# Kernel tuning notes

Hardware: AMD Instinct MI355X
Metric: run time of the kernel (lower is better)

The kernel has to match this reference:

```python
import jax, jax.numpy as jnp
import numpy as np

NS = 100000; NT = 100000; M = 512; D = 256; DL = 128; H = 4; C = 256; K = 64
ITERS = 50; POS_MARGIN = 0.1


def conv1(w, b, x):
    # 1x1 Conv1d: x (B, Cin, N), w (Cout, Cin)
    return jnp.einsum('oi,bin->bon', w, x) + b[None, :, None]


def attn_block(p, x, src):
    # attentional propagation: MHA message + MLP([x, msg]) (residual added by caller)
    wq, bq, wk, bk, wv, bv, wm, bm, w1, b1, w2, b2 = p
    B, Dm, N = x.shape
    Dh = Dm // H
    Nm = src.shape[2]
    q = conv1(wq, bq, x).reshape(B, H, Dh, N)
    k = conv1(wk, bk, src).reshape(B, H, Dh, Nm)
    v = conv1(wv, bv, src).reshape(B, H, Dh, Nm)
    a = jax.nn.softmax(jnp.einsum('bhdn,bhdm->bhnm', q, k) * (1.0 / np.sqrt(Dh)), axis=-1)
    msg = jnp.einsum('bhnm,bhdm->bhdn', a, v).reshape(B, Dm, N)
    msg = conv1(wm, bm, msg)
    h = jax.nn.relu(conv1(w1, b1, jnp.concatenate([x, msg], axis=1)))
    return conv1(w2, b2, h)


def nn_id(points, nodes):
    # 1-NN node id per point; points (N,3), nodes (M,3)
    d = (jnp.sum(points * points, 1, keepdims=True) - 2.0 * points @ nodes.T
         + jnp.sum(nodes * nodes, 1)[None, :])
    return jnp.argmin(d, axis=1)


def build_patches(pcd_id, m, k):
    # grouping_wrapper: first k point indices assigned to each node, -1 padded
    n = pcd_id.shape[0]
    order = jnp.argsort(pcd_id)  # stable
    sid = pcd_id[order]
    starts = jnp.searchsorted(sid, jnp.arange(m))
    rank = jnp.arange(n) - starts[sid]
    patch = jnp.full((m, k), -1, jnp.int32)
    patch = patch.at[sid, rank].set(order.astype(jnp.int32), mode='drop')  # rank>=k dropped
    mask = (patch < 0).astype(jnp.float32)
    return jnp.where(patch < 0, 0, patch), mask


def log_optimal_transport(scores, alpha, iters):
    b, m, n = scores.shape
    bins0 = jnp.full((b, m, 1), alpha)
    bins1 = jnp.full((b, 1, n), alpha)
    corner = jnp.full((b, 1, 1), alpha)
    Z = jnp.concatenate([jnp.concatenate([scores, bins0], 2),
                         jnp.concatenate([bins1, corner], 2)], 1)
    norm = -np.log(m + n)
    log_mu = jnp.concatenate([jnp.full((m,), norm, jnp.float32), jnp.array([np.log(n) + norm], jnp.float32)])
    log_nu = jnp.concatenate([jnp.full((n,), norm, jnp.float32), jnp.array([np.log(m) + norm], jnp.float32)])
    log_mu = jnp.broadcast_to(log_mu, (b, m + 1))
    log_nu = jnp.broadcast_to(log_nu, (b, n + 1))

    def body(carry, _):
        u, v = carry
        u = log_mu - jax.nn.logsumexp(Z + v[:, None, :], axis=2)
        v = log_nu - jax.nn.logsumexp(Z + u[:, :, None], axis=1)
        return (u, v), None

    (u, v), _ = jax.lax.scan(body, (jnp.zeros((b, m + 1)), jnp.zeros((b, n + 1))), None, length=iters)
    return Z + u[:, :, None] + v[:, None, :] - norm


def rpmnet_sinkhorn(log_alpha, bins0, bins1, iters):
    b = log_alpha.shape[0]
    corner = jnp.zeros((b, 1, 1), log_alpha.dtype)
    la = jnp.concatenate([jnp.concatenate([log_alpha, bins0], 2),
                          jnp.concatenate([bins1, corner], 2)], 1)

    def body(la, _):
        row = la - jax.nn.logsumexp(la, axis=2, keepdims=True)
        la = jnp.concatenate([row[:, :-1, :], la[:, -1:, :]], axis=1)  # normalize all rows but slack
        col = la - jax.nn.logsumexp(la, axis=1, keepdims=True)
        la = jnp.concatenate([col[:, :, :-1], la[:, :, -1:]], axis=2)  # normalize all cols but slack
        return la, None

    la, _ = jax.lax.scan(body, la, None, length=iters)
    return la


def _forward(src_pcd_c, tgt_pcd_c, src_node_c, tgt_node_c, src_feats_c, tgt_feats_c,
             src_final_f, tgt_final_f, rot, trans, src_pcd_raw, tgt_pcd_raw,
             c_wq, c_bq, c_wk, c_bk, c_wv, c_bv, c_wm, c_bm, c_w1, c_b1, c_w2, c_b2,
             l_wq, l_bq, l_wk, l_bk, l_wv, l_bv, l_wm, l_bm, l_w1, l_b1, l_w2, l_b2,
             fp_w, fp_b, lfp_w, lfp_b, bin_score, node_corr):
    # KNN assignment + patch grouping (irregular gather/scatter)
    src_patch, src_mask = build_patches(nn_id(src_pcd_c, src_node_c), M, K)
    tgt_patch, tgt_mask = build_patches(nn_id(tgt_pcd_c, tgt_node_c), M, K)
    # coarse attention stack (self, cross, self) with residuals
    cp = lambda i: (c_wq[i], c_bq[i], c_wk[i], c_bk[i], c_wv[i], c_bv[i], c_wm[i], c_bm[i],
                    c_w1[i], c_b1[i], c_w2[i], c_b2[i])
    sf, tf = src_feats_c, tgt_feats_c
    sf = sf + attn_block(cp(0), sf, sf); tf = tf + attn_block(cp(0), tf, tf)
    sf = sf + attn_block(cp(1), sf, tf); tf = tf + attn_block(cp(1), tf, sf)  # sequential, like torch
    sf = sf + attn_block(cp(2), sf, sf); tf = tf + attn_block(cp(2), tf, tf)
    sf = conv1(fp_w, fp_b, sf); tf = conv1(fp_w, fp_b, tf)
    scores = jnp.einsum('bdn,bdm->bnm', sf, tf) / np.sqrt(D)
    scores = log_optimal_transport(scores, bin_score, ITERS)
    # correspondence-driven patch gather
    sn = node_corr[:, 0]; tn = node_corr[:, 1]
    src_sel = src_patch[sn].reshape(-1)
    tgt_sel = tgt_patch[tn].reshape(-1)
    smask = src_mask[sn]; tmask = tgt_mask[tn]  # (C,K)
    # GT local scores (training path)
    src_raw_t = (rot @ src_pcd_raw.T + trans).T
    sc = src_raw_t[src_sel].reshape(C, K, 3)
    tc = tgt_pcd_raw[tgt_sel].reshape(C, K, 3)
    d2 = jnp.maximum(jnp.sum(sc * sc, -1)[:, :, None] + jnp.sum(tc * tc, -1)[:, None, :]
                     - 2.0 * jnp.einsum('cnd,cmd->cnm', sc, tc), 0.0)
    gt = (jnp.sqrt(d2) < POS_MARGIN).astype(jnp.float32)
    row = jnp.maximum(1.0 - jnp.sum(gt, -1), 0.0)[:, :, None]
    col = jnp.maximum(1.0 - jnp.sum(gt, -2), 0.0)[:, None, :]
    col = jnp.concatenate([col, jnp.zeros((C, 1, 1), jnp.float32)], -1)
    gt = jnp.concatenate([jnp.concatenate([gt, row], -1), col], -2)  # (C,K+1,K+1)
    gt = gt.at[:, :-1, :].multiply(1.0 - smask[:, :, None])
    gt = gt.at[:, :, :-1].multiply(1.0 - tmask[:, None, :])
    # local patch features + attention stack
    spf = src_final_f[src_sel].reshape(C, K, DL).transpose(0, 2, 1)  # (C,DL,K)
    tpf = tgt_final_f[tgt_sel].reshape(C, K, DL).transpose(0, 2, 1)
    lp = lambda i: (l_wq[i], l_bq[i], l_wk[i], l_bk[i], l_wv[i], l_bv[i], l_wm[i], l_bm[i],
                    l_w1[i], l_b1[i], l_w2[i], l_b2[i])
    spf = spf + attn_block(lp(0), spf, spf); tpf = tpf + attn_block(lp(0), tpf, tpf)
    spf = spf + attn_block(lp(1), spf, tpf); tpf = tpf + attn_block(lp(1), tpf, spf)
    spf = spf + attn_block(lp(2), spf, spf); tpf = tpf + attn_block(lp(2), tpf, tpf)
    spf = conv1(lfp_w, lfp_b, spf); tpf = conv1(lfp_w, lfp_b, tpf)
    ls = jnp.einsum('bdn,bdm->bnm', spf, tpf) / np.sqrt(DL)
    ls = jnp.where(smask[:, :, None] > 0, -1e6, ls)
    ls = jnp.where(tmask[:, None, :] > 0, -1e6, ls)
    ls = rpmnet_sinkhorn(ls, jnp.zeros((C, K, 1), jnp.float32), jnp.zeros((C, 1, K), jnp.float32), ITERS)
    return scores, ls, gt


def setup_inputs() -> dict:
    key = jax.random.key(0)
    ks = jax.random.split(key, 48)

    def rn(i, shape, scale):
        return jax.random.normal(ks[i], shape, jnp.float32) * scale

    inp = {}
    inp['src_pcd_c'] = jax.random.uniform(ks[0], (NS, 3), jnp.float32)
    inp['tgt_pcd_c'] = jax.random.uniform(ks[1], (NT, 3), jnp.float32)
    inp['src_node_c'] = jax.random.uniform(ks[2], (M, 3), jnp.float32)
    inp['tgt_node_c'] = jax.random.uniform(ks[3], (M, 3), jnp.float32)
    inp['src_feats_c'] = rn(4, (1, D, M), 1.0)
    inp['tgt_feats_c'] = rn(5, (1, D, M), 1.0)
    inp['src_final_f'] = rn(6, (NS, DL), 1.0)
    inp['tgt_final_f'] = rn(7, (NT, DL), 1.0)
    inp['rot'] = jnp.eye(3, dtype=jnp.float32)
    inp['trans'] = jnp.zeros((3, 1), jnp.float32)
    inp['src_pcd_raw'] = jax.random.uniform(ks[8], (NS, 3), jnp.float32)
    inp['tgt_pcd_raw'] = jax.random.uniform(ks[9], (NT, 3), jnp.float32)
    inp['node_corr'] = jax.random.randint(ks[10], (C, 2), 0, M)
    i = 11
    for pre, d in (('c_', D), ('l_', DL)):
        for nm in ('wq', 'wk', 'wv', 'wm'):
            inp[pre + nm] = rn(i, (3, d, d), 1.0 / np.sqrt(d)); i += 1
            inp[pre + 'b' + nm[1]] = jnp.zeros((3, d), jnp.float32)
        inp[pre + 'w1'] = rn(i, (3, 2 * d, 2 * d), 1.0 / np.sqrt(2 * d)); i += 1
        inp[pre + 'b1'] = jnp.zeros((3, 2 * d), jnp.float32)
        inp[pre + 'w2'] = rn(i, (3, d, 2 * d), 1.0 / np.sqrt(2 * d)); i += 1
        inp[pre + 'b2'] = jnp.zeros((3, d), jnp.float32)
    inp['fp_w'] = rn(i, (D, D), 1.0 / np.sqrt(D)); i += 1
    inp['fp_b'] = jnp.zeros((D,), jnp.float32)
    inp['lfp_w'] = rn(i, (DL, DL), 1.0 / np.sqrt(DL)); i += 1
    inp['lfp_b'] = jnp.zeros((DL,), jnp.float32)
    inp['bin_score'] = jnp.ones((), jnp.float32)
    return inp


def reference(src_pcd_c, tgt_pcd_c, src_node_c, tgt_node_c, src_feats_c, tgt_feats_c,
              src_final_f, tgt_final_f, rot, trans, src_pcd_raw, tgt_pcd_raw,
              c_wq, c_bq, c_wk, c_bk, c_wv, c_bv, c_wm, c_bm, c_w1, c_b1, c_w2, c_b2,
              l_wq, l_bq, l_wk, l_bk, l_wv, l_bv, l_wm, l_bm, l_w1, l_b1, l_w2, l_b2,
              fp_w, fp_b, lfp_w, lfp_b, bin_score, node_corr):
    return _forward(src_pcd_c, tgt_pcd_c, src_node_c, tgt_node_c, src_feats_c, tgt_feats_c,
                    src_final_f, tgt_final_f, rot, trans, src_pcd_raw, tgt_pcd_raw,
                    c_wq, c_bq, c_wk, c_bk, c_wv, c_bv, c_wm, c_bm, c_w1, c_b1, c_w2, c_b2,
                    l_wq, l_bq, l_wk, l_bk, l_wv, l_bv, l_wm, l_bm, l_w1, l_b1, l_w2, l_b2,
                    fp_w, fp_b, lfp_w, lfp_b, bin_score, node_corr)
```

## Files before the change

kernel.cpp:

```cpp
#include <hip/hip_runtime.h>
#include <math.h>

static constexpr int NODES = 512;
static constexpr int CC    = 256;
static constexpr int KP    = 64;
static constexpr int ZDIM  = 513;
static constexpr int TPNB  = 16;
static constexpr int TPROWS = 33;

typedef unsigned short u16;
typedef short bf16x8 __attribute__((ext_vector_type(8)));
typedef float f32x4 __attribute__((ext_vector_type(4)));

__device__ __forceinline__ u16 f2b(float f){
  unsigned u = __float_as_uint(f);
  unsigned r = (u + 0x7FFF + ((u >> 16) & 1)) >> 16;
  return (u16)r;
}
__device__ __forceinline__ float b2f(u16 h){ return __uint_as_float(((unsigned)h) << 16); }
__device__ __forceinline__ f32x4 mfma16(bf16x8 a, bf16x8 b, f32x4 c){
  return __builtin_amdgcn_mfma_f32_16x16x32_bf16(a, b, c, 0, 0, 0);
}
__device__ __forceinline__ void astore(float* p, float v){
  __hip_atomic_store(p, v, __ATOMIC_RELAXED, __HIP_MEMORY_SCOPE_AGENT);
}
__device__ __forceinline__ float fpoll(const float* p){
  const unsigned* up = (const unsigned*)p;
  unsigned v = __hip_atomic_load(up, __ATOMIC_RELAXED, __HIP_MEMORY_SCOPE_AGENT);
  while (v == 0xFFFFFFFFu){
    __builtin_amdgcn_s_sleep(1);
    v = __hip_atomic_load(up, __ATOMIC_RELAXED, __HIP_MEMORY_SCOPE_AGENT);
  }
  return __uint_as_float(v);
}
__device__ __forceinline__ void fpoll2(const float* p0, const float* p1,
                                       float* a, float* b){
  const unsigned* u0 = (const unsigned*)p0;
  const unsigned* u1 = (const unsigned*)p1;
  unsigned x = __hip_atomic_load(u0, __ATOMIC_RELAXED, __HIP_MEMORY_SCOPE_AGENT);
  unsigned y = __hip_atomic_load(u1, __ATOMIC_RELAXED, __HIP_MEMORY_SCOPE_AGENT);
  while (x == 0xFFFFFFFFu || y == 0xFFFFFFFFu){
    __builtin_amdgcn_s_sleep(1);
    if (x == 0xFFFFFFFFu) x = __hip_atomic_load(u0, __ATOMIC_RELAXED, __HIP_MEMORY_SCOPE_AGENT);
    if (y == 0xFFFFFFFFu) y = __hip_atomic_load(u1, __ATOMIC_RELAXED, __HIP_MEMORY_SCOPE_AGENT);
  }
  *a = __uint_as_float(x); *b = __uint_as_float(y);
}

static constexpr int NBW = (2539520 + 255) / 256;

__global__ __launch_bounds__(256) void prep(
  const float* cwq, const float* cwk, const float* cwv, const float* cwm,
  const float* cw1, const float* cw2, const float* fpw,
  const float* lwq, const float* lwk, const float* lwv, const float* lwm,
  const float* lw1, const float* lw2, const float* lfp, u16* __restrict__ dst,
  const float* __restrict__ pts_s, int ns, const float* __restrict__ nodes_s,
  int* __restrict__ id_s, int* __restrict__ hist_s,
  const float* __restrict__ pts_t, int ntt, const float* __restrict__ nodes_t,
  int* __restrict__ id_t, int* __restrict__ hist_t, int nbs, int nbnn,
  const float* __restrict__ fs, const float* __restrict__ ft,
  u16* __restrict__ cf, float* __restrict__ cff)
{
  int blk = blockIdx.x;
  int t = threadIdx.x;
  if (blk < NBW){
    int i = blk*256 + t;
    if (i >= 2539520) return;
    const float* s; int off;
    if      (i <  196608){ s=cwq; off=0; }
    else if (i <  393216){ s=cwk; off=196608; }
    else if (i <  589824){ s=cwv; off=393216; }
    else if (i <  786432){ s=cwm; off=589824; }
    else if (i < 1572864){ s=cw1; off=786432; }
    else if (i < 1966080){ s=cw2; off=1572864; }
    else if (i < 2031616){ s=fpw; off=1966080; }
    else if (i < 2080768){ s=lwq; off=2031616; }
    else if (i < 2129920){ s=lwk; off=2080768; }
    else if (i < 2179072){ s=lwv; off=2129920; }
    else if (i < 2228224){ s=lwm; off=2179072; }
    else if (i < 2424832){ s=lw1; off=2228224; }
    else if (i < 2523136){ s=lw2; off=2424832; }
    else                 { s=lfp; off=2523136; }
    dst[i] = f2b(s[i - off]);
    return;
  }
  if (blk < NBW + nbnn){
#pragma clang fp contract(off)
    __shared__ float nx[NODES], ny[NODES], nz[NODES], nn[NODES];
    __shared__ int h[NODES];
    int b2 = blk - NBW;
    const float* pts; const float* nodes; int* out; int* hist; int n; int bb;
    if (b2 < nbs){ pts=pts_s; nodes=nodes_s; out=id_s; hist=hist_s; n=ns; bb=b2; }
    else         { pts=pts_t; nodes=nodes_t; out=id_t; hist=hist_t; n=ntt; bb=b2-nbs; }
    for (int m = t; m < NODES; m += 256){
      float a = nodes[m*3+0], b = nodes[m*3+1], c = nodes[m*3+2];
      nx[m]=a; ny[m]=b; nz[m]=c;
      nn[m] = a*a + b*b + c*c;
      h[m] = 0;
    }
// ... 280 lines not shown
    f32x4 acc = {};
    const u16* wrow = W2 + (long)(o0+lr)*512 + 8*lk;
#pragma unroll
    for (int ks = 0; ks < 16; ++ks){
      bf16x8 b = *(const bf16x8*)(wrow + ks*32);
      bf16x8 av = *(const bf16x8*)(&h1[lr*512 + ((ks*32 + 8*lk) ^ ((lr&7)<<3))]);
      acc = mfma16(av, b, acc);
    }
    int col = o0 + lr; float bb = b2[col];
#pragma unroll
    for (int q_ = 0; q_ < 4; ++q_){
      long idx = (long)(lk*4+q_)*256 + col;
      float v = acc[q_] + bb + xf[idx];
      xf[idx] = v;
      x[idx] = f2b(v);
    }
  }
}

__global__ __launch_bounds__(256) void coarse_proj(
    const u16* __restrict__ cf, const u16* __restrict__ W,
    const float* __restrict__ bias, u16* __restrict__ out)
{
  int z = blockIdx.x;
  int side = z >> 4, slice = z & 15;
  const u16* in = cf + (long)side*131072;
  u16* o = out + (long)side*131072;
  int n0 = slice << 5;
  int wv_ = threadIdx.x >> 6, L = threadIdx.x & 63, lr = L & 15, lk = L >> 4;
  const u16* inb = in + (long)(n0 + lr)*256 + 8*lk;
  for (int oi = 0; oi < 4; ++oi){
    int o0 = (wv_*4 + oi) << 4;
    const u16* wrow = W + (long)(o0 + lr)*256 + 8*lk;
    f32x4 acc[2] = {};
#pragma unroll
    for (int ks = 0; ks < 8; ++ks){
      bf16x8 b = *(const bf16x8*)(wrow + ks*32);
#pragma unroll
      for (int a = 0; a < 2; ++a){
        bf16x8 av = *(const bf16x8*)(inb + a*16*256 + ks*32);
        acc[a] = mfma16(av, b, acc[a]);
      }
    }
    int col = o0 + lr; float bb = bias[col];
#pragma unroll
    for (int a = 0; a < 2; ++a)
#pragma unroll
      for (int q_ = 0; q_ < 4; ++q_)
        o[(long)(n0 + a*16 + lk*4 + q_)*256 + col] = f2b(acc[a][q_] + bb);
  }
}

__global__ __launch_bounds__(256) void coarse_scores(
    const u16* __restrict__ sfp, const u16* __restrict__ tfp,
    float* __restrict__ Z, float* __restrict__ Zt)
{
  int n0 = blockIdx.y << 6, m0 = blockIdx.x << 6;
  int wv_ = threadIdx.x >> 6, L = threadIdx.x & 63, lr = L & 15, lk = L >> 4;
  f32x4 acc[4] = {};
  const u16* arow = sfp + (long)(n0 + lr)*256 + 8*lk;
  const u16* brow = tfp + (long)(m0 + wv_*16 + lr)*256 + 8*lk;
#pragma unroll
  for (int ks = 0; ks < 8; ++ks){
    bf16x8 b = *(const bf16x8*)(brow + ks*32);
#pragma unroll
    for (int a = 0; a < 4; ++a){
      bf16x8 av = *(const bf16x8*)(arow + a*16*256 + ks*32);
      acc[a] = mfma16(av, b, acc[a]);
    }
  }
  int col = m0 + wv_*16 + lr;
#pragma unroll
  for (int a = 0; a < 4; ++a)
#pragma unroll
    for (int q_ = 0; q_ < 4; ++q_){
      int row = n0 + a*16 + lk*4 + q_;
      float v = acc[a][q_]*0.0625f;
      Z[(long)row*513 + col] = v;
      Zt[(long)col*513 + row] = v;
    }
}

__global__ __launch_bounds__(256) void fill_border(float* Z, float* Zt,
                                                   const float* __restrict__ alpha)
{
  int i = blockIdx.x*256 + threadIdx.x;
  if (i < ZDIM){
    float a = alpha[0];
    Z[(long)i*ZDIM + (ZDIM-1)] = a;
    Z[(long)(ZDIM-1)*ZDIM + i] = a;
    Zt[(long)i*ZDIM + (ZDIM-1)] = a;
    Zt[(long)(ZDIM-1)*ZDIM + i] = a;
  }
}

static constexpr int ARENA = 142336;

__device__ void transport_role(char* arena, int bid,
    const float* __restrict__ Z, const float* __restrict__ Zt,
    float* Rr, float* Cc, float* UU, float* VV,
    float* __restrict__ out, float outadd)
{
  float* A = (float*)arena;
  float* B = A + TPROWS*513;
  float* RrL = B + TPROWS*513;
  float* CcL = RrL + 513;
  float* M   = CcL + 513;
  float* rown = M + 513;
  float* cown = rown + TPROWS;
  float* uown = cown + TPROWS;
  int tid = threadIdx.x;
  int wv_ = tid >> 6, lane = tid & 63;
  int r0 = bid * TPROWS;
  int nr = 513 - r0; if (nr > TPROWS) nr = TPROWS;

  for (int i = wv_; i < nr; i += 8){
    const float* zr  = Z  + (long)(r0+i)*513;
    const float* ztr = Zt + (long)(r0+i)*513;
    for (int j = lane; j < 513; j += 64){ A[i*513+j] = zr[j]; B[i*513+j] = ztr[j]; }
  }
  __syncthreads();
  for (int i = wv_; i < nr; i += 8){
    float m = -INFINITY;
    for (int j = lane; j < 513; j += 64) m = fmaxf(m, A[i*513+j]);
    for (int o = 32; o; o >>= 1) m = fmaxf(m, __shfl_xor(m, o));
    if (lane == 0){ rown[i] = m; astore(&Rr[r0+i], m); }
  }
  if (tid == 0)      fpoll2(&Rr[0], &Rr[512], &RrL[0], &RrL[512]);
  else if (tid < 512) RrL[tid] = fpoll(&Rr[tid]);
  __syncthreads();
  for (int i = wv_; i < nr; i += 8){
    float m = -INFINITY;
    for (int j = lane; j < 513; j += 64) m = fmaxf(m, B[i*513+j] - RrL[j]);
    for (int o = 32; o; o >>= 1) m = fmaxf(m, __shfl_xor(m, o));
    if (lane == 0){ cown[i] = m; astore(&Cc[r0+i], m); }
  }
  if (tid == 0)      fpoll2(&Cc[0], &Cc[512], &CcL[0], &CcL[512]);
  else if (tid < 512) CcL[tid] = fpoll(&Cc[tid]);
  __syncthreads();
  for (int i = wv_; i < nr; i += 8){
    float ro = rown[i], co = cown[i];
    for (int j = lane; j < 513; j += 64){
      A[i*513+j] = __expf(A[i*513+j] - ro - CcL[j]);
      B[i*513+j] = __expf(B[i*513+j] - co - RrL[j]);
    }
  }
  __syncthreads();
  const float EBM = 1.0f/1024.0f, EBL = 0.5f;
  for (int i = wv_; i < nr; i += 8){
    float s = 0.f;
    for (int j = lane; j < 513; j += 64) s += A[i*513+j];
    for (int o = 32; o; o >>= 1) s += __shfl_xor(s, o);
    if (lane == 0){
      int r = r0+i; float u = ((r < 512) ? EBM : EBL) / s;
      uown[i] = u; astore(&UU[r], u);
    }
  }
  for (int it = 0; it < 50; ++it){
    const float* src = &UU[(long)it*640];
    if (tid == 0)      fpoll2(&src[0], &src[512], &M[0], &M[512]);
    else if (tid < 512) M[tid] = fpoll(&src[tid]);
    __syncthreads();
    for (int i = wv_; i < nr; i += 8){
      float s = 0.f;
      for (int j = lane; j < 513; j += 64) s = fmaf(B[i*513+j], M[j], s);
      for (int o = 32; o; o >>= 1) s += __shfl_xor(s, o);
      if (lane == 0){
        int r = r0+i;
        astore(&VV[(long)it*640 + r], ((r < 512) ? EBM : EBL) / s);
      }
    }
    __syncthreads();
    if (it == 49) break;
    const float* srcv = &VV[(long)it*640];
    if (tid == 0)      fpoll2(&srcv[0], &srcv[512], &M[0], &M[512]);
    else if (tid < 512) M[tid] = fpoll(&srcv[tid]);
    __syncthreads();
    for (int i = wv_; i < nr; i += 8){
      float s = 0.f;
      for (int j = lane; j < 513; j += 64) s = fmaf(A[i*513+j], M[j], s);
      for (int o = 32; o; o >>= 1) s += __shfl_xor(s, o);
      if (lane == 0){
        int r = r0+i; float u = ((r < 512) ? EBM : EBL) / s;
        uown[i] = u; astore(&UU[(long)(it+1)*640 + r], u);
      }
    }
    __syncthreads();
  }
  {
    const float* srcv = &VV[49L*640];
    if (tid == 0)      fpoll2(&srcv[0], &srcv[512], &M[0], &M[512]);
    else if (tid < 512) M[tid] = fpoll(&srcv[tid]);
  }
  __syncthreads();
  for (int j = tid; j < 513; j += 512) M[j] = __logf(M[j]) - CcL[j];
  __syncthreads();
  for (int i = wv_; i < nr; i += 8){
    int r = r0 + i;
    float uu = __logf(uown[i]) - rown[i];
    const float* zr = Z + (long)r*513;
    float* orow = out + (long)r*513;
    for (int j = lane; j < 513; j += 64) orow[j] = zr[j] + uu + M[j] + outadd;
  }
}

__device__ void layerapp(
    u16* __restrict__ x, const u16* __restrict__ s, u16* __restrict__ pool,
    const u16* __restrict__ Wq, const u16* __restrict__ Wk,
    const u16* __restrict__ Wv, const u16* __restrict__ Wm,
    const u16* __restrict__ W1, const u16* __restrict__ W2,
    const float* __restrict__ bq, const float* __restrict__ bk,
    const float* __restrict__ bv, const float* __restrict__ bm,
    const float* __restrict__ b1, const float* __restrict__ b2)
{
  int tid = threadIdx.x;
  int wv8 = tid >> 6, L = tid & 63, lr = L & 15, lk = L >> 4;
  u16* qS = pool; u16* kS = pool + 8192; u16* vT = pool + 16384; u16* msgS = pool + 24832;
  int swr = (lr & 7) << 3;

#pragma unroll
  for (int proj = 0; proj < 3; ++proj){
    const u16* in = proj ? s : x;
    const u16* W = proj==0?Wq:proj==1?Wk:Wv;
    const float* bi = proj==0?bq:proj==1?bk:bv;
    int o0 = wv8 << 4;
    f32x4 acc[4] = {};
    const u16* wrow = W + (long)(o0+lr)*128 + 8*lk;
    const u16* inr = in + (long)lr*128 + 8*lk;
#pragma unroll
    for (int ks = 0; ks < 4; ++ks){
      bf16x8 b = *(const bf16x8*)(wrow + ks*32);
#pragma unroll
      for (int a = 0; a < 4; ++a){
        bf16x8 av = *(const bf16x8*)(inr + a*16*128 + ks*32);
        acc[a] = mfma16(av, b, acc[a]);
      }
    }
    int col = o0 + lr; float bb = bi[col];
    if (proj < 2){
      u16* dst = (proj==0 ? qS : kS);
#pragma unroll
      for (int a = 0; a < 4; ++a)
#pragma unroll
        for (int q_ = 0; q_ < 4; ++q_){
          int row = a*16 + lk*4 + q_;
          dst[row*128 + (col ^ ((row&7)<<3))] = f2b(acc[a][q_] + bb);
        }
    } else {
#pragma unroll
      for (int a = 0; a < 4; ++a)
#pragma unroll
        for (int q_ = 0; q_ < 4; ++q_)
          vT[col*66 + a*16 + lk*4 + q_] = f2b(acc[a][q_] + bb);
    }
  }
  __syncthreads();
  int h = wv8 >> 1, half = wv8 & 1;
  bf16x8 qf[2], kf[4];
#pragma unroll
  for (int ai = 0; ai < 2; ++ai){
    int a = half*2 + ai;
    qf[ai] = *(const bf16x8*)(&qS[(a*16+lr)*128 + ((h*32 + 8*lk) ^ swr)]);
  }
#pragma unroll
  for (int b = 0; b < 4; ++b)
    kf[b] = *(const bf16x8*)(&kS[(b*16+lr)*128 + ((h*32 + 8*lk) ^ swr)]);
  f32x4 sc[2][4] = {};
#pragma unroll
  for (int b = 0; b < 4; ++b)
#pragma unroll
    for (int ai = 0; ai < 2; ++ai)
      sc[ai][b] = mfma16(qf[ai], kf[b], sc[ai][b]);
  const float SCs = 0.17677669529663687f;
  float invs[2][4];
#pragma unroll
  for (int ai = 0; ai < 2; ++ai)
#pragma unroll
    for (int q_ = 0; q_ < 4; ++q_){
      float m = sc[ai][0][q_];
#pragma unroll
      for (int b = 1; b < 4; ++b) m = fmaxf(m, sc[ai][b][q_]);
      m = fmaxf(m, __shfl_xor(m, 1)); m = fmaxf(m, __shfl_xor(m, 2));
      m = fmaxf(m, __shfl_xor(m, 4)); m = fmaxf(m, __shfl_xor(m, 8));
      float ss = 0.f;
#pragma unroll
      for (int b = 0; b < 4; ++b){
        float e = __expf((sc[ai][b][q_] - m)*SCs);
// ... 27 lines not shown
        bf16x8 av = *(const bf16x8*)(&P[(a*16+lr)*64 + ((ks*32 + 8*lk) ^ swr)]);
        mv[ai][bt] = mfma16(av, bf, mv[ai][bt]);
      }
    }
#pragma unroll
  for (int ai = 0; ai < 2; ++ai){
    int a = half*2 + ai;
#pragma unroll
    for (int bt = 0; bt < 2; ++bt)
#pragma unroll
      for (int q_ = 0; q_ < 4; ++q_){
        int row = a*16 + lk*4 + q_;
        msgS[row*128 + ((h*32 + bt*16 + lr) ^ ((row&7)<<3))] = f2b(mv[ai][bt][q_]);
      }
  }
  __syncthreads();
  u16* m2 = pool;
  {
    int o0 = wv8 << 4;
    f32x4 acc[4] = {};
    const u16* wrow = Wm + (long)(o0+lr)*128 + 8*lk;
#pragma unroll
    for (int ks = 0; ks < 4; ++ks){
      bf16x8 b = *(const bf16x8*)(wrow + ks*32);
#pragma unroll
      for (int a = 0; a < 4; ++a){
        bf16x8 av = *(const bf16x8*)(&msgS[(a*16+lr)*128 + ((ks*32 + 8*lk) ^ swr)]);
        acc[a] = mfma16(av, b, acc[a]);
      }
    }
    int col = o0+lr; float bb = bm[col];
#pragma unroll
    for (int a = 0; a < 4; ++a)
#pragma unroll
      for (int q_ = 0; q_ < 4; ++q_){
        int row = a*16+lk*4+q_;
        m2[row*128 + (col ^ ((row&7)<<3))] = f2b(acc[a][q_] + bb);
      }
  }
  __syncthreads();
  u16* h1 = pool + 8192;
#pragma unroll
  for (int oi = 0; oi < 2; ++oi){
    int o0 = (wv8*2 + oi) << 4;
    f32x4 acc[4] = {};
    const u16* wrow = W1 + (long)(o0+lr)*256 + 8*lk;
#pragma unroll
    for (int ks = 0; ks < 8; ++ks){
      int kk = ks*32;
      bf16x8 b = *(const bf16x8*)(wrow + kk);
#pragma unroll
      for (int a = 0; a < 4; ++a){
        bf16x8 av;
        if (kk < 128) av = *(const bf16x8*)(x + (long)(a*16+lr)*128 + kk + 8*lk);
        else          av = *(const bf16x8*)(&m2[(a*16+lr)*128 + ((kk - 128 + 8*lk) ^ swr)]);
        acc[a] = mfma16(av, b, acc[a]);
      }
    }
    int col = o0+lr; float bb = b1[col];
#pragma unroll
    for (int a = 0; a < 4; ++a)
#pragma unroll
      for (int q_ = 0; q_ < 4; ++q_){
        int row = a*16+lk*4+q_;
        h1[row*256 + (col ^ ((row&7)<<3))] = f2b(fmaxf(acc[a][q_] + bb, 0.f));
      }
  }
  __syncthreads();
  {
    int o0 = wv8 << 4;
    f32x4 acc[4] = {};
    const u16* wrow = W2 + (long)(o0+lr)*256 + 8*lk;
#pragma unroll
    for (int ks = 0; ks < 8; ++ks){
      bf16x8 b = *(const bf16x8*)(wrow + ks*32);
#pragma unroll
      for (int a = 0; a < 4; ++a){
        bf16x8 av = *(const bf16x8*)(&h1[(a*16+lr)*256 + ((ks*32 + 8*lk) ^ swr)]);
        acc[a] = mfma16(av, b, acc[a]);
      }
    }
    int col = o0+lr; float bb = b2[col];
#pragma unroll
    for (int a = 0; a < 4; ++a)
#pragma unroll
      for (int q_ = 0; q_ < 4; ++q_){
        int ri = (a*16+lk*4+q_)*128 + col;
        x[ri] = f2b(acc[a][q_] + bb + b2f(x[ri]));
      }
  }
  __syncthreads();
}

__device__ void gt_role(char* arena, int c,
    const float* __restrict__ sraw, const float* __restrict__ traw,
    const float* __restrict__ rot, const float* __restrict__ trans,
    const int* __restrict__ patch_s, const int* __restrict__ patch_t,
    const int* __restrict__ corr,
    const int* __restrict__ cnt_s, const int* __restrict__ cnt_t,
    float* __restrict__ out)
{
#pragma clang fp contract(off)
  float* sx = (float*)arena;         float* sy = sx + 64;
  float* sz = sy + 64;               float* spp = sz + 64;
  float* txa = spp + 64;             float* tya = txa + 64;
  float* tza = tya + 64;             float* tpp = tza + 64;
  float* g   = tpp + 64;
  float* rowsum = g + 64*65;
  float* colsum = rowsum + 64;
  int tid = threadIdx.x;
  int sn = corr[c*2], tn = corr[c*2+1];
  int cs = cnt_s[sn], ct = cnt_t[tn];
  if (tid < 64){
    int idx = patch_s[sn*KP + tid];
    float p0 = sraw[(long)idx*3], p1 = sraw[(long)idx*3+1], p2 = sraw[(long)idx*3+2];
    float a0 = fmaf(rot[2], p2, fmaf(rot[1], p1, rot[0]*p0)) + trans[0];
    float a1 = fmaf(rot[5], p2, fmaf(rot[4], p1, rot[3]*p0)) + trans[1];
    float a2 = fmaf(rot[8], p2, fmaf(rot[7], p1, rot[6]*p0)) + trans[2];
    sx[tid]=a0; sy[tid]=a1; sz[tid]=a2;
    spp[tid] = a0*a0 + a1*a1 + a2*a2;
  } else if (tid < 128){
    int l = tid - 64;
    int idx = patch_t[tn*KP + l];
    float p0 = traw[(long)idx*3], p1 = traw[(long)idx*3+1], p2 = traw[(long)idx*3+2];
    txa[l]=p0; tya[l]=p1; tza[l]=p2;
    tpp[l] = p0*p0 + p1*p1 + p2*p2;
  }
  __syncthreads();
  for (int e = tid; e < 4096; e += 512){
    int n = e >> 6, m = e & 63;
    float dot = fmaf(sz[n], tza[m], fmaf(sy[n], tya[m], sx[n]*txa[m]));
    float d2 = (spp[n] + tpp[m]) - 2.0f*dot;
    d2 = fmaxf(d2, 0.f);
    g[n*65 + m] = (sqrtf(d2) < 0.1f) ? 1.f : 0.f;
  }
  __syncthreads();
  if (tid < 64){
    float s = 0.f;
    for (int m = 0; m < 64; ++m) s += g[tid*65 + m];
    rowsum[tid] = fmaxf(1.f - s, 0.f);
// ... 2 lines not shown
    float s = 0.f;
    for (int n = 0; n < 64; ++n) s += g[n*65 + m];
    colsum[m] = fmaxf(1.f - s, 0.f);
  }
  __syncthreads();
  float* o = out + (long)c*4225;
  for (int e = tid; e < 4225; e += 512){
    int r = e / 65, col = e % 65;
    float v;
    if (r < 64 && col < 64) v = g[r*65 + col];
    else if (r < 64)        v = rowsum[r];
    else if (col < 64)      v = colsum[col];
    else                    v = 0.f;
    if (r < 64 && r >= cs)    v = 0.f;
    if (col < 64 && col >= ct) v = 0.f;
    o[e] = v;
  }
}

__device__ void local_role(char* arena, int c,
    const float* __restrict__ Fs, const float* __restrict__ Ft,
    const int* __restrict__ patch_s, const int* __restrict__ patch_t,
    const int* __restrict__ corr,
    const int* __restrict__ cnt_s, const int* __restrict__ cnt_t,
    const u16* WlQ, const u16* WlK, const u16* WlV, const u16* WlM,
    const u16* Wl1, const u16* Wl2, const u16* Wlfp,
    const float* lbq, const float* lbk, const float* lbv, const float* lbm,
    const float* lb1, const float* lb2, const float* lfpB,
    float* __restrict__ out_ls)
{
  u16* X    = (u16*)arena;
  u16* pool = (u16*)(arena + 32768);
  float* LA = (float*)(arena + 98816);
  float* ET = (float*)(arena + 115976);
  float* uvec = (float*)(arena + 133136);
  float* vvec = (float*)(arena + 133456);
  float* u0s  = (float*)(arena + 133776);
  float* Ul   = (float*)(arena + 134096);
  float* Vl   = (float*)(arena + 134416);
  int* sel    = (int*)(arena + 134736);
  int tid = threadIdx.x;
  int wv8 = tid >> 6, L = tid & 63, lr = L & 15, lk = L >> 4;
  int swr = (lr & 7) << 3;

  if (tid < 128){
    int side = tid >> 6, n = tid & 63;
    int node = corr[c*2 + side];
    sel[tid] = (side ? patch_t : patch_s)[node*KP + n];
  }
  __syncthreads();
  for (int e = tid; e < 16384; e += 512){
    int side = e >> 13, r = e & 8191, n = r >> 7, d = r & 127;
    const float* F = side ? Ft : Fs;
    X[e] = f2b(F[(long)sel[side*64 + n]*128 + d]);
  }
  __syncthreads();

  for (int l = 0; l < 3; ++l){
    const u16* wq = WlQ + (size_t)l*16384; const u16* wk = WlK + (size_t)l*16384;
    const u16* wv = WlV + (size_t)l*16384; const u16* wm = WlM + (size_t)l*16384;
    const u16* w1 = Wl1 + (size_t)l*65536; const u16* w2 = Wl2 + (size_t)l*32768;
    const float* bq = lbq + (size_t)l*128; const float* bk = lbk + (size_t)l*128;
    const float* bv = lbv + (size_t)l*128; const float* bm = lbm + (size_t)l*128;
    const float* b1 = lb1 + (size_t)l*256; const float* b2 = lb2 + (size_t)l*128;
    int cross = (l == 1);
    layerapp(X,        X + (cross ? 8192 : 0), pool, wq,wk,wv,wm,w1,w2, bq,bk,bv,bm,b1,b2);
    layerapp(X + 8192, X + (cross ? 0 : 8192), pool, wq,wk,wv,wm,w1,w2, bq,bk,bv,bm,b1,b2);
  }

  u16* sp = pool; u16* tp = pool + 8192;
  for (int u_ = wv8; u_ < 16; u_ += 8){
    int sideSel = u_ >> 3, ot = u_ & 7;
    const u16* in = X + sideSel*8192;
    u16* dst = sideSel ? tp : sp;
    int o0 = ot << 4;
    f32x4 acc[4] = {};
    const u16* wrow = Wlfp + (long)(o0+lr)*128 + 8*lk;
    const u16* inr = in + (long)lr*128 + 8*lk;
#pragma unroll
    for (int ks = 0; ks < 4; ++ks){
      bf16x8 b = *(const bf16x8*)(wrow + ks*32);
#pragma unroll
      for (int a = 0; a < 4; ++a){
        bf16x8 av = *(const bf16x8*)(inr + a*16*128 + ks*32);
        acc[a] = mfma16(av, b, acc[a]);
      }
    }
    int col = o0 + lr; float bb = lfpB[col];
#pragma unroll
    for (int a = 0; a < 4; ++a)
#pragma unroll
      for (int q_ = 0; q_ < 4; ++q_){
        int row = a*16 + lk*4 + q_;
        dst[row*128 + (col ^ ((row&7)<<3))] = f2b(acc[a][q_] + bb);
      }
  }
  __syncthreads();

  int cs = cnt_s[corr[c*2]], ct = cnt_t[corr[c*2+1]];
  for (int t_ = wv8; t_ < 16; t_ += 8){
    int mt = t_ >> 2, nt = t_ & 3;
    f32x4 acc = {};
#pragma unroll
    for (int ks = 0; ks < 4; ++ks){
      bf16x8 a = *(const bf16x8*)(&sp[(mt*16 + lr)*128 + ((ks*32 + 8*lk) ^ swr)]);
      bf16x8 b = *(const bf16x8*)(&tp[(nt*16 + lr)*128 + ((ks*32 + 8*lk) ^ swr)]);
      acc = mfma16(a, b, acc);
    }
    const float SCS = 0.08838834764831845f;
#pragma unroll
    for (int q_ = 0; q_ < 4; ++q_){
      int row = mt*16 + lk*4 + q_;
      int col = nt*16 + lr;
      float v = acc[q_] * SCS;
      if (row >= cs || col >= ct) v = -1000000.0f;
      LA[row*66 + col] = v;
    }
  }
  if (tid < 65){ LA[64*66 + tid] = 0.f; LA[tid*66 + 64] = 0.f; uvec[tid] = 1.f; vvec[tid] = 1.f; }
  __syncthreads();

  float* E = (float*)pool;
  int g = tid >> 3, sub = tid & 7;
  {
    float mx = -INFINITY;
    for (int j = sub; j < 65; j += 8) mx = fmaxf(mx, LA[g*66 + j]);
    mx = fmaxf(mx, __shfl_xor(mx, 1)); mx = fmaxf(mx, __shfl_xor(mx, 2));
    mx = fmaxf(mx, __shfl_xor(mx, 4));
    float s = 0.f;
    for (int j = sub; j < 65; j += 8) s += __expf(LA[g*66 + j] - mx);
    s += __shfl_xor(s, 1); s += __shfl_xor(s, 2); s += __shfl_xor(s, 4);
    float u0 = mx + __logf(s);
    if (sub == 0) u0s[g] = u0;
    for (int j = sub; j < 65; j += 8){
      float e = __expf(LA[g*66 + j] - u0);
      E[g*66 + j] = e;
      ET[j*66 + g] = e;
    }
  }
  if (tid < 65){
    E[64*66 + tid] = 1.f;
    ET[tid*66 + 64] = 1.f;
    if (tid == 64) u0s[64] = 0.f;
  }
  __syncthreads();
  for (int it = 0; it < 50; ++it){
    {
      float s = 0.f;
      for (int r = sub; r < 65; r += 8) s = fmaf(ET[g*66 + r], uvec[r], s);
      s += __shfl_xor(s, 1); s += __shfl_xor(s, 2); s += __shfl_xor(s, 4);
      if (sub == 0) vvec[g] = 1.f / s;
    }
    __syncthreads();
    if (it == 49) break;
    {
      float s = 0.f;
      for (int j = sub; j < 65; j += 8) s = fmaf(E[g*66 + j], vvec[j], s);
      s += __shfl_xor(s, 1); s += __shfl_xor(s, 2); s += __shfl_xor(s, 4);
      if (sub == 0) uvec[g] = 1.f / s;
    }
    __syncthreads();
  }
  __syncthreads();
  if (tid < 65){ Ul[tid] = u0s[tid] - __logf(uvec[tid]); Vl[tid] = -__logf(vvec[tid]); }
  __syncthreads();
  for (int e = tid; e < 4225; e += 512){
    int r = e / 65, c2 = e % 65;
    out_ls[(long)c*4225 + e] = LA[r*66 + c2] - Ul[r] - Vl[c2];
  }
}

__global__ __launch_bounds__(512) void mega(
    const float* Z, const float* Zt, float* Rr, float* Cc, float* UU, float* VV,
    float* out0, float outadd,
    const float* Fs, const float* Ft,
    const int* patch_s, const int* patch_t, const int* corr,
    const int* cnt_s, const int* cnt_t,
    const u16* WlQ, const u16* WlK, const u16* WlV, const u16* WlM,
    const u16* Wl1, const u16* Wl2, const u16* Wlfp,
    const float* lbq, const float* lbk, const float* lbv, const float* lbm,
    const float* lb1, const float* lb2, const float* lfpB,
    float* out_ls,
    const float* sraw, const float* traw, const float* rot, const float* trans,
    float* out_gt)
{
  __shared__ __align__(16) char arena[ARENA];
  int b = blockIdx.x;
  if (b < 128){
    if ((b & 7) == 0)
      transport_role(arena, b >> 3, Z, Zt, Rr, Cc, UU, VV, out0, outadd);
    return;
  }
  b -= 128;
  local_role(arena, b, Fs, Ft, patch_s, patch_t, corr, cnt_s, cnt_t,
             WlQ, WlK, WlV, WlM, Wl1, Wl2, Wlfp,
             lbq, lbk, lbv, lbm, lb1, lb2, lfpB, out_ls);
  gt_role(arena, b, sraw, traw, rot, trans,
          patch_s, patch_t, corr, cnt_s, cnt_t, out_gt);
}

extern "C" void kernel_launch(void* const* d_in, const int* in_sizes, int n_in,
                              void* d_out, int out_size, void* d_ws, size_t ws_size,
                              hipStream_t stream)
{
  const float* src_pcd_c  = (const float*)d_in[0];
  const float* tgt_pcd_c  = (const float*)d_in[1];
  const float* src_node_c = (const float*)d_in[2];
  const float* tgt_node_c = (const float*)d_in[3];
  const float* src_feats  = (const float*)d_in[4];
  const float* tgt_feats  = (const float*)d_in[5];
  const float* src_final  = (const float*)d_in[6];
  const float* tgt_final  = (const float*)d_in[7];
  const float* rot        = (const float*)d_in[8];
  const float* trans      = (const float*)d_in[9];
  const float* src_raw    = (const float*)d_in[10];
  const float* tgt_raw    = (const float*)d_in[11];
  const int*   node_corr  = (const int*)d_in[12];
  const float* c_wq = (const float*)d_in[13]; const float* c_bq = (const float*)d_in[14];
  const float* c_wk = (const float*)d_in[15]; const float* c_bk = (const float*)d_in[16];
  const float* c_wv = (const float*)d_in[17]; const float* c_bv = (const float*)d_in[18];
  const float* c_wm = (const float*)d_in[19]; const float* c_bm = (const float*)d_in[20];
  const float* c_w1 = (const float*)d_in[21]; const float* c_b1 = (const float*)d_in[22];
  const float* c_w2 = (const float*)d_in[23]; const float* c_b2 = (const float*)d_in[24];
  const float* l_wq = (const float*)d_in[25]; const float* l_bq = (const float*)d_in[26];
  const float* l_wk = (const float*)d_in[27]; const float* l_bk = (const float*)d_in[28];
  const float* l_wv = (const float*)d_in[29]; const float* l_bv = (const float*)d_in[30];
  const float* l_wm = (const float*)d_in[31]; const float* l_bm = (const float*)d_in[32];
  const float* l_w1 = (const float*)d_in[33]; const float* l_b1 = (const float*)d_in[34];
  const float* l_w2 = (const float*)d_in[35]; const float* l_b2 = (const float*)d_in[36];
  const float* fp_w = (const float*)d_in[37]; const float* fp_b = (const float*)d_in[38];
  const float* lfp_w = (const float*)d_in[39]; const float* lfp_b = (const float*)d_in[40];
  const float* bin_score = (const float*)d_in[41];

  const int NS = in_sizes[0] / 3;
  const int NT = in_sizes[1] / 3;

  float* FB = (float*)d_ws;
  size_t off = 0;
  auto falloc = [&](size_t n){ float* p = FB + off; off += (n + 63) & ~size_t(63); return p; };
  float* Zx  = falloc(263169);
  float* Zt  = falloc(263169);
  float* Rr  = falloc(640);
  float* Cc  = falloc(640);
  float* UU  = falloc(32000);
  float* VV  = falloc(32000);
  float* cff = falloc(262144);
  u16* cf   = (u16*)falloc(131072);
  u16* qb   = (u16*)falloc(131072);
  u16* kb   = (u16*)falloc(131072);
  u16* vtb  = (u16*)falloc(131072);
  u16* msgb = (u16*)falloc(131072);
  u16* sfpb = (u16*)falloc(131072);
  u16* wsb  = (u16*)falloc(1269760);

  int* IB = (int*)(FB + off);
  size_t ioff = 0;
  auto ialloc = [&](size_t n){ int* p = IB + ioff; ioff += (n + 63) & ~size_t(63); return p; };
  int* id_s = ialloc(NS);
  int* id_t = ialloc(NT);
  const int nbs = (NS + 255) / 256, nbt = (NT + 255) / 256;
  int* hist_s = ialloc((size_t)nbs * NODES);
  int* hist_t = ialloc((size_t)nbt * NODES);
  int* cnt_s = ialloc(NODES);
  int* cnt_t = ialloc(NODES);
  int* patch_s = ialloc(NODES*KP);
  int* patch_t = ialloc(NODES*KP);

  float* out0 = (float*)d_out;
  float* out_ls = out0 + ZDIM*ZDIM;
  float* out_gt = out_ls + (long)CC*65*65;

  u16* WcQ = wsb + 0;
  u16* WcK = wsb + 196608;
  u16* WcV = wsb + 393216;
  u16* WcM = wsb + 589824;
  u16* Wc1 = wsb + 786432;
  u16* Wc2 = wsb + 1572864;
  u16* Wfp = wsb + 1966080;
  u16* WlQ = wsb + 2031616;
  u16* WlK = wsb + 2080768;
  u16* WlV = wsb + 2129920;
  u16* WlM = wsb + 2179072;
  u16* Wl1 = wsb + 2228224;
  u16* Wl2 = wsb + 2424832;
  u16* Wlfp = wsb + 2523136;

  hipMemsetAsync(Rr, 0xFF, (640 + 640 + 32000 + 32000)*sizeof(float), stream);
  hipMemsetAsync(patch_s, 0, NODES*KP*sizeof(int), stream);
  hipMemsetAsync(patch_t, 0, NODES*KP*sizeof(int), stream);

  int nbnn = nbs + nbt;
  prep<<<NBW + nbnn + 1024, 256, 0, stream>>>(
      c_wq, c_wk, c_wv, c_wm, c_w1, c_w2, fp_w,
      l_wq, l_wk, l_wv, l_wm, l_w1, l_w2, lfp_w, wsb,
      src_pcd_c, NS, src_node_c, id_s, hist_s,
      tgt_pcd_c, NT, tgt_node_c, id_t, hist_t, nbs, nbnn,
      src_feats, tgt_feats, cf, cff);
  scan_kernel2<<<256, 256, 0, stream>>>(hist_s, nbs, cnt_s, hist_t, nbt, cnt_t);
  rank_kernel<<<nbs + nbt, 256, 0, stream>>>(
      id_s, NS, hist_s, patch_s, id_t, NT, hist_t, patch_t, nbs);

  int crossL[3] = {0, 1, 0};
  for (int l = 0; l < 3; ++l){
    u16* wq = WcQ + (size_t)l*65536; u16* wk = WcK + (size_t)l*65536;
    u16* wv = WcV + (size_t)l*65536; u16* wm = WcM + (size_t)l*65536;
    u16* w1 = Wc1 + (size_t)l*262144; u16* w2 = Wc2 + (size_t)l*131072;
    const float* bq = c_bq + (size_t)l*256; const float* bk = c_bk + (size_t)l*256;
    const float* bv = c_bv + (size_t)l*256; const float* bm = c_bm + (size_t)l*256;
    const float* b1 = c_b1 + (size_t)l*512; const float* b2 = c_b2 + (size_t)l*256;
    if (!crossL[l]){
      coarse_qkv<<<96, 256, 0, stream>>>(cf, 0, 0, wq, wk, wv, bq, bk, bv, qb, kb, vtb);
      coarse_attn<<<128, 256, 0, stream>>>(qb, kb, vtb, msgb, 0);
      coarse_ffn<<<64, 256, 0, stream>>>(msgb, cf, cff, wm, bm, w1, b1, w2, b2, 0);
    } else {
      for (int sd = 0; sd < 2; ++sd){
        coarse_qkv<<<48, 256, 0, stream>>>(cf, 1, sd, wq, wk, wv, bq, bk, bv, qb, kb, vtb);
        coarse_attn<<<64, 256, 0, stream>>>(qb, kb, vtb, msgb, sd);
        coarse_ffn<<<32, 256, 0, stream>>>(msgb, cf, cff, wm, bm, w1, b1, w2, b2, sd);
      }
    }
  }
  coarse_proj<<<32, 256, 0, stream>>>(cf, Wfp, fp_b, sfpb);
  coarse_scores<<<dim3(8,8), 256, 0, stream>>>(sfpb, sfpb + 131072, Zx, Zt);
  fill_border<<<3, 256, 0, stream>>>(Zx, Zt, bin_score);

  mega<<<128 + CC, 512, 0, stream>>>(
      Zx, Zt, Rr, Cc, UU, VV, out0, logf(1024.0f),
      src_final, tgt_final, patch_s, patch_t, node_corr, cnt_s, cnt_t,
      WlQ, WlK, WlV, WlM, Wl1, Wl2, Wlfp,
      l_bq, l_bk, l_bv, l_bm, l_b1, l_b2, lfp_b,
      out_ls,
      src_raw, tgt_raw, rot, trans, out_gt);

  (void)n_in; (void)out_size; (void)ws_size;
}
```

Baseline: 842.6 us.

## Restructure Sinkhorn transport to row-partitioned blocks with partial column reductions

```diff
diff --git a/kernel.cpp b/kernel.cpp
--- a/kernel.cpp
+++ b/kernel.cpp
@@ -5,8 +5,8 @@
 static constexpr int CC    = 256;
 static constexpr int KP    = 64;
 static constexpr int ZDIM  = 513;
-static constexpr int TPNB  = 16;
-static constexpr int TPROWS = 33;
+static constexpr int TPNB  = 8;
+static constexpr int TPROWS = 65;
 
 typedef unsigned short u16;
 typedef short bf16x8 __attribute__((ext_vector_type(8)));
@@ -32,19 +32,6 @@
     v = __hip_atomic_load(up, __ATOMIC_RELAXED, __HIP_MEMORY_SCOPE_AGENT);
   }
   return __uint_as_float(v);
-}
-__device__ __forceinline__ void fpoll2(const float* p0, const float* p1,
-                                       float* a, float* b){
-  const unsigned* u0 = (const unsigned*)p0;
-  const unsigned* u1 = (const unsigned*)p1;
-  unsigned x = __hip_atomic_load(u0, __ATOMIC_RELAXED, __HIP_MEMORY_SCOPE_AGENT);
-  unsigned y = __hip_atomic_load(u1, __ATOMIC_RELAXED, __HIP_MEMORY_SCOPE_AGENT);
-  while (x == 0xFFFFFFFFu || y == 0xFFFFFFFFu){
-    __builtin_amdgcn_s_sleep(1);
-    if (x == 0xFFFFFFFFu) x = __hip_atomic_load(u0, __ATOMIC_RELAXED, __HIP_MEMORY_SCOPE_AGENT);
-    if (y == 0xFFFFFFFFu) y = __hip_atomic_load(u1, __ATOMIC_RELAXED, __HIP_MEMORY_SCOPE_AGENT);
-  }
-  *a = __uint_as_float(x); *b = __uint_as_float(y);
 }
 
 static constexpr int NBW = (2539520 + 255) / 256;
@@ -431,8 +418,7 @@
 }
 
 __global__ __launch_bounds__(256) void coarse_scores(
-    const u16* __restrict__ sfp, const u16* __restrict__ tfp,
-    float* __restrict__ Z, float* __restrict__ Zt)
+    const u16* __restrict__ sfp, const u16* __restrict__ tfp, float* __restrict__ Z)
 {
   int n0 = blockIdx.y << 6, m0 = blockIdx.x << 6;
   int wv_ = threadIdx.x >> 6, L = threadIdx.x & 63, lr = L & 15, lk = L >> 4;
@@ -452,77 +438,63 @@
 #pragma unroll
   for (int a = 0; a < 4; ++a)
 #pragma unroll
-    for (int q_ = 0; q_ < 4; ++q_){
-      int row = n0 + a*16 + lk*4 + q_;
-      float v = acc[a][q_]*0.0625f;
-      Z[(long)row*513 + col] = v;
-      Zt[(long)col*513 + row] = v;
-    }
-}
-
-__global__ __launch_bounds__(256) void fill_border(float* Z, float* Zt,
-                                                   const float* __restrict__ alpha)
+    for (int q_ = 0; q_ < 4; ++q_)
+      Z[(long)(n0 + a*16 + lk*4 + q_)*513 + col] = acc[a][q_]*0.0625f;
+}
+
+__global__ __launch_bounds__(256) void fill_border(float* Z, const float* __restrict__ alpha)
 {
   int i = blockIdx.x*256 + threadIdx.x;
   if (i < ZDIM){
     float a = alpha[0];
     Z[(long)i*ZDIM + (ZDIM-1)] = a;
     Z[(long)(ZDIM-1)*ZDIM + i] = a;
-    Zt[(long)i*ZDIM + (ZDIM-1)] = a;
-    Zt[(long)(ZDIM-1)*ZDIM + i] = a;
   }
 }
 
 static constexpr int ARENA = 142336;
 
 __device__ void transport_role(char* arena, int bid,
-    const float* __restrict__ Z, const float* __restrict__ Zt,
-    float* Rr, float* Cc, float* UU, float* VV,
+    const float* __restrict__ Z, float* PM, float* PV,
     float* __restrict__ out, float outadd)
 {
-  float* A = (float*)arena;
-  float* B = A + TPROWS*513;
-  float* RrL = B + TPROWS*513;
-  float* CcL = RrL + 513;
-  float* M   = CcL + 513;
+  float* A    = (float*)arena;
+  float* CcL  = A + TPROWS*513;
+  float* M    = CcL + 513;
   float* rown = M + 513;
-  float* cown = rown + TPROWS;
-  float* uown = cown + TPROWS;
+  float* uL   = rown + TPROWS;
   int tid = threadIdx.x;
   int wv_ = tid >> 6, lane = tid & 63;
   int r0 = bid * TPROWS;
   int nr = 513 - r0; if (nr > TPROWS) nr = TPROWS;
 
   for (int i = wv_; i < nr; i += 8){
-    const float* zr  = Z  + (long)(r0+i)*513;
-    const float* ztr = Zt + (long)(r0+i)*513;
-    for (int j = lane; j < 513; j += 64){ A[i*513+j] = zr[j]; B[i*513+j] = ztr[j]; }
+    const float* zr = Z + (long)(r0+i)*513;
+    for (int j = lane; j < 513; j += 64) A[i*513+j] = zr[j];
   }
   __syncthreads();
   for (int i = wv_; i < nr; i += 8){
     float m = -INFINITY;
     for (int j = lane; j < 513; j += 64) m = fmaxf(m, A[i*513+j]);
     for (int o = 32; o; o >>= 1) m = fmaxf(m, __shfl_xor(m, o));
-    if (lane == 0){ rown[i] = m; astore(&Rr[r0+i], m); }
-  }
-  if (tid == 0)      fpoll2(&Rr[0], &Rr[512], &RrL[0], &RrL[512]);
-  else if (tid < 512) RrL[tid] = fpoll(&Rr[tid]);
+    if (lane == 0) rown[i] = m;
+  }
+  __syncthreads();
+  for (int r = tid; r < 513; r += 512){
+    float m = -INFINITY;
+    for (int i = 0; i < nr; ++i) m = fmaxf(m, A[i*513+r] - rown[i]);
+    astore(&PM[bid*640 + r], m);
+  }
+  for (int r = tid; r < 513; r += 512){
+    float m = -INFINITY;
+    for (int b = 0; b < TPNB; ++b) m = fmaxf(m, fpoll(&PM[b*640 + r]));
+    CcL[r] = m;
+  }
   __syncthreads();
   for (int i = wv_; i < nr; i += 8){
-    float m = -INFINITY;
-    for (int j = lane; j < 513; j += 64) m = fmaxf(m, B[i*513+j] - RrL[j]);
-    for (int o = 32; o; o >>= 1) m = fmaxf(m, __shfl_xor(m, o));
-    if (lane == 0){ cown[i] = m; astore(&Cc[r0+i], m); }
-  }
-  if (tid == 0)      fpoll2(&Cc[0], &Cc[512], &CcL[0], &CcL[512]);
-  else if (tid < 512) CcL[tid] = fpoll(&Cc[tid]);
-  __syncthreads();
-  for (int i = wv_; i < nr; i += 8){
-    float ro = rown[i], co = cown[i];
-    for (int j = lane; j < 513; j += 64){
+    float ro = rown[i];
+    for (int j = lane; j < 513; j += 64)
       A[i*513+j] = __expf(A[i*513+j] - ro - CcL[j]);
-      B[i*513+j] = __expf(B[i*513+j] - co - RrL[j]);
-    }
   }
   __syncthreads();
   const float EBM = 1.0f/1024.0f, EBL = 0.5f;
@@ -530,53 +502,37 @@
     float s = 0.f;
     for (int j = lane; j < 513; j += 64) s += A[i*513+j];
     for (int o = 32; o; o >>= 1) s += __shfl_xor(s, o);
-    if (lane == 0){
-      int r = r0+i; float u = ((r < 512) ? EBM : EBL) / s;
-      uown[i] = u; astore(&UU[r], u);
-    }
-  }
+    if (lane == 0){ int r = r0+i; uL[i] = ((r < 512) ? EBM : EBL) / s; }
+  }
+  __syncthreads();
   for (int it = 0; it < 50; ++it){
-    const float* src = &UU[(long)it*640];
-    if (tid == 0)      fpoll2(&src[0], &src[512], &M[0], &M[512]);
-    else if (tid < 512) M[tid] = fpoll(&src[tid]);
+    float* slot = PV + (long)it * (TPNB*640);
+    for (int r = tid; r < 513; r += 512){
+      float pv = 0.f;
+      for (int i = 0; i < nr; ++i) pv = fmaf(A[i*513+r], uL[i], pv);
+      astore(&slot[bid*640 + r], pv);
+    }
+    for (int r = tid; r < 513; r += 512){
+      float s = 0.f;
+      for (int b = 0; b < TPNB; ++b) s += fpoll(&slot[b*640 + r]);
+      M[r] = ((r < 512) ? EBM : EBL) / s;
+    }
     __syncthreads();
-    for (int i = wv_; i < nr; i += 8){
-      float s = 0.f;
-      for (int j = lane; j < 513; j += 64) s = fmaf(B[i*513+j], M[j], s);
-      for (int o = 32; o; o >>= 1) s += __shfl_xor(s, o);
-      if (lane == 0){
-        int r = r0+i;
-        astore(&VV[(long)it*640 + r], ((r < 512) ? EBM : EBL) / s);
-      }
-    }
-    __syncthreads();
-    if (it == 49) break;
-    const float* srcv = &VV[(long)it*640];
-    if (tid == 0)      fpoll2(&srcv[0], &srcv[512], &M[0], &M[512]);
-    else if (tid < 512) M[tid] = fpoll(&srcv[tid]);
-    __syncthreads();
-    for (int i = wv_; i < nr; i += 8){
-      float s = 0.f;
-      for (int j = lane; j < 513; j += 64) s = fmaf(A[i*513+j], M[j], s);
-      for (int o = 32; o; o >>= 1) s += __shfl_xor(s, o);
-      if (lane == 0){
-        int r = r0+i; float u = ((r < 512) ? EBM : EBL) / s;
-        uown[i] = u; astore(&UU[(long)(it+1)*640 + r], u);
-      }
-    }
-    __syncthreads();
-  }
-  {
-    const float* srcv = &VV[49L*640];
-    if (tid == 0)      fpoll2(&srcv[0], &srcv[512], &M[0], &M[512]);
-    else if (tid < 512) M[tid] = fpoll(&srcv[tid]);
-  }
-  __syncthreads();
+    if (it < 49){
+      for (int i = wv_; i < nr; i += 8){
+        float s = 0.f;
+        for (int j = lane; j < 513; j += 64) s = fmaf(A[i*513+j], M[j], s);
+        for (int o = 32; o; o >>= 1) s += __shfl_xor(s, o);
+        if (lane == 0){ int r = r0+i; uL[i] = ((r < 512) ? EBM : EBL) / s; }
+      }
+      __syncthreads();
+    }
+  }
   for (int j = tid; j < 513; j += 512) M[j] = __logf(M[j]) - CcL[j];
   __syncthreads();
   for (int i = wv_; i < nr; i += 8){
     int r = r0 + i;
-    float uu = __logf(uown[i]) - rown[i];
+    float uu = __logf(uL[i]) - rown[i];
     const float* zr = Z + (long)r*513;
     float* orow = out + (long)r*513;
     for (int j = lane; j < 513; j += 64) orow[j] = zr[j] + uu + M[j] + outadd;
@@ -605,13 +561,12 @@
     int o0 = wv8 << 4;
     f32x4 acc[4] = {};
     const u16* wrow = W + (long)(o0+lr)*128 + 8*lk;
-    const u16* inr = in + (long)lr*128 + 8*lk;
 #pragma unroll
     for (int ks = 0; ks < 4; ++ks){
       bf16x8 b = *(const bf16x8*)(wrow + ks*32);
 #pragma unroll
       for (int a = 0; a < 4; ++a){
-        bf16x8 av = *(const bf16x8*)(inr + a*16*128 + ks*32);
+        bf16x8 av = *(const bf16x8*)(in + (a*16+lr)*128 + ((ks*32 + 8*lk) ^ swr));
         acc[a] = mfma16(av, b, acc[a]);
       }
     }
@@ -745,7 +700,7 @@
 #pragma unroll
       for (int a = 0; a < 4; ++a){
         bf16x8 av;
-        if (kk < 128) av = *(const bf16x8*)(x + (long)(a*16+lr)*128 + kk + 8*lk);
+        if (kk < 128) av = *(const bf16x8*)(x + (a*16+lr)*128 + ((kk + 8*lk) ^ swr));
         else          av = *(const bf16x8*)(&m2[(a*16+lr)*128 + ((kk - 128 + 8*lk) ^ swr)]);
         acc[a] = mfma16(av, b, acc[a]);
       }
@@ -778,7 +733,8 @@
     for (int a = 0; a < 4; ++a)
 #pragma unroll
       for (int q_ = 0; q_ < 4; ++q_){
-        int ri = (a*16+lk*4+q_)*128 + col;
+        int row = a*16+lk*4+q_;
+        int ri = row*128 + (col ^ ((row&7)<<3));
         x[ri] = f2b(acc[a][q_] + bb + b2f(x[ri]));
       }
   }
@@ -887,7 +843,7 @@
   for (int e = tid; e < 16384; e += 512){
     int side = e >> 13, r = e & 8191, n = r >> 7, d = r & 127;
     const float* F = side ? Ft : Fs;
-    X[e] = f2b(F[(long)sel[side*64 + n]*128 + d]);
+    X[side*8192 + n*128 + (d ^ ((n&7)<<3))] = f2b(F[(long)sel[side*64 + n]*128 + d]);
   }
   __syncthreads();
 
@@ -911,13 +867,12 @@
     int o0 = ot << 4;
     f32x4 acc[4] = {};
     const u16* wrow = Wlfp + (long)(o0+lr)*128 + 8*lk;
-    const u16* inr = in + (long)lr*128 + 8*lk;
 #pragma unroll
     for (int ks = 0; ks < 4; ++ks){
       bf16x8 b = *(const bf16x8*)(wrow + ks*32);
 #pragma unroll
       for (int a = 0; a < 4; ++a){
-        bf16x8 av = *(const bf16x8*)(inr + a*16*128 + ks*32);
+        bf16x8 av = *(const bf16x8*)(in + (a*16+lr)*128 + ((ks*32 + 8*lk) ^ swr));
         acc[a] = mfma16(av, b, acc[a]);
       }
     }
@@ -1006,7 +961,7 @@
 }
 
 __global__ __launch_bounds__(512) void mega(
-    const float* Z, const float* Zt, float* Rr, float* Cc, float* UU, float* VV,
+    const float* Z, float* PM, float* PV,
     float* out0, float outadd,
     const float* Fs, const float* Ft,
     const int* patch_s, const int* patch_t, const int* corr,
@@ -1022,8 +977,8 @@
   __shared__ __align__(16) char arena[ARENA];
   int b = blockIdx.x;
   if (b < 128){
-    if ((b & 7) == 0)
-      transport_role(arena, b >> 3, Z, Zt, Rr, Cc, UU, VV, out0, outadd);
+    if ((b & 15) == 0)
+      transport_role(arena, b >> 4, Z, PM, PV, out0, outadd);
     return;
   }
   b -= 128;
@@ -1074,11 +1029,8 @@
   size_t off = 0;
   auto falloc = [&](size_t n){ float* p = FB + off; off += (n + 63) & ~size_t(63); return p; };
   float* Zx  = falloc(263169);
-  float* Zt  = falloc(263169);
-  float* Rr  = falloc(640);
-  float* Cc  = falloc(640);
-  float* UU  = falloc(32000);
-  float* VV  = falloc(32000);
+  float* PM  = falloc(TPNB*640);
+  float* PV  = falloc(50*TPNB*640);
   float* cff = falloc(262144);
   u16* cf   = (u16*)falloc(131072);
   u16* qb   = (u16*)falloc(131072);
@@ -1120,7 +1072,7 @@
   u16* Wl2 = wsb + 2424832;
   u16* Wlfp = wsb + 2523136;
 
-  hipMemsetAsync(Rr, 0xFF, (640 + 640 + 32000 + 32000)*sizeof(float), stream);
+  hipMemsetAsync(PM, 0xFF, (TPNB*640 + 50*TPNB*640)*sizeof(float), stream);
   hipMemsetAsync(patch_s, 0, NODES*KP*sizeof(int), stream);
   hipMemsetAsync(patch_t, 0, NODES*KP*sizeof(int), stream);
 
@@ -1156,11 +1108,11 @@
     }
   }
   coarse_proj<<<32, 256, 0, stream>>>(cf, Wfp, fp_b, sfpb);
-  coarse_scores<<<dim3(8,8), 256, 0, stream>>>(sfpb, sfpb + 131072, Zx, Zt);
-  fill_border<<<3, 256, 0, stream>>>(Zx, Zt, bin_score);
+  coarse_scores<<<dim3(8,8), 256, 0, stream>>>(sfpb, sfpb + 131072, Zx);
+  fill_border<<<3, 256, 0, stream>>>(Zx, bin_score);
 
   mega<<<128 + CC, 512, 0, stream>>>(
-      Zx, Zt, Rr, Cc, UU, VV, out0, logf(1024.0f),
+      Zx, PM, PV, out0, logf(1024.0f),
       src_final, tgt_final, patch_s, patch_t, node_corr, cnt_s, cnt_t,
       WlQ, WlK, WlV, WlM, Wl1, Wl2, Wlfp,
       l_bq, l_bk, l_bv, l_bm, l_b1, l_b2, lfp_b,
```

Measured after the change: 1.166 ms. +38.4%, slower.
